# Optimization experiments

Measured on AMD Instinct MI355X. Metric: run time of the kernel, lower is better.

## Reference

```python
import jax, jax.numpy as jnp
import numpy as np

DIM = 1024
HEADS = 16
DIM_HEAD = 64
SCALE = DIM_HEAD ** -0.5
LN_EPS = 1e-5


def layer_norm(x, g, b):
    mu = jnp.mean(x, axis=-1, keepdims=True)
    var = jnp.mean(jnp.square(x - mu), axis=-1, keepdims=True)
    return (x - mu) * jax.lax.rsqrt(var + LN_EPS) * g + b


def setup_inputs() -> dict:
    key = jax.random.key(0)
    ks = jax.random.split(key, 8)
    w_std = DIM ** -0.5  # keep GEMM outputs O(1)
    return {
        "query": jax.random.normal(ks[0], (4, 512, DIM), jnp.float32),
        "kv": jax.random.normal(ks[1], (4, 2048, DIM), jnp.float32),
        "ln_q_g": jnp.ones((DIM,), jnp.float32),
        "ln_q_b": jnp.zeros((DIM,), jnp.float32),
        "ln_kv_g": jnp.ones((DIM,), jnp.float32),
        "ln_kv_b": jnp.zeros((DIM,), jnp.float32),
        "Wq": jax.random.normal(ks[2], (DIM, DIM), jnp.float32) * w_std,
        "bq": jnp.zeros((DIM,), jnp.float32),
        "Wk": jax.random.normal(ks[3], (DIM, DIM), jnp.float32) * w_std,
        "bk": jnp.zeros((DIM,), jnp.float32),
        "Wv": jax.random.normal(ks[4], (DIM, DIM), jnp.float32) * w_std,
        "bv": jnp.zeros((DIM,), jnp.float32),
        "Wo": jax.random.normal(ks[5], (DIM, DIM), jnp.float32) * w_std,
        "bo": jnp.zeros((DIM,), jnp.float32),
    }


def reference(query, kv, ln_q_g, ln_q_b, ln_kv_g, ln_kv_b,
              Wq, bq, Wk, bk, Wv, bv, Wo, bo):
    kv_n = layer_norm(kv, ln_kv_g, ln_kv_b)            # (b, n_kv, d)
    residual = query
    q_n = layer_norm(query, ln_q_g, ln_q_b)            # (b, n_q, d)

    q = q_n @ Wq + bq                                   # (b, n_q, inner)
    kv_input = jnp.concatenate((kv_n, q_n), axis=-2)    # (b, n_kv+n_q, d)
    k = kv_input @ Wk + bk
    v = kv_input @ Wv + bv

    def split_heads(t):
        b, n, _ = t.shape
        return t.reshape(b, n, HEADS, DIM_HEAD).transpose(0, 2, 1, 3)  # b h n dh

    q = split_heads(q) * SCALE
    k = split_heads(k)
    v = split_heads(v)

    sim = jnp.einsum('bhid,bhjd->bhij', q, k)           # (b, h, n_q, n_kv+n_q)
    sim = sim - jax.lax.stop_gradient(jnp.max(sim, axis=-1, keepdims=True))
    attn = jax.nn.softmax(sim, axis=-1)
    out = jnp.einsum('bhij,bhjd->bhid', attn, v)        # (b, h, n_q, dh)

    b, h, n, dh = out.shape
    out = out.transpose(0, 2, 1, 3).reshape(b, n, h * dh)
    return out @ Wo + bo + residual
```

## Files before the change

### kernel.cpp

```cpp
#include <hip/hip_runtime.h>
#include <hip/hip_bf16.h>

#define B_    4
#define NQ    512
#define NKV   2048
#define NT    2560
#define DIM_  1024
#define HEADS 16
#define DH    64
#define NSEQT 10240
#define SCALE_Q_L2E 0.18033688011112042f

typedef short bf16x8 __attribute__((ext_vector_type(8)));
typedef float f32x4  __attribute__((ext_vector_type(4)));
typedef __hip_bfloat16 bf16;

__device__ inline void gll16(const bf16* g, bf16* l) {
  __builtin_amdgcn_global_load_lds(
      (const __attribute__((address_space(1))) unsigned int*)g,
      (__attribute__((address_space(3))) unsigned int*)l, 16, 0, 0);
}

#define VMCNT(n) asm volatile("s_waitcnt vmcnt(" #n ")" ::: "memory")
#define BAR() __builtin_amdgcn_s_barrier()

__global__ __launch_bounds__(256) void prep_kernel(
    const float* __restrict__ query, const float* __restrict__ kv,
    const float* __restrict__ lgq, const float* __restrict__ lbq,
    const float* __restrict__ lgkv, const float* __restrict__ lbkv,
    bf16* __restrict__ X,
    const float* __restrict__ W0, const float* __restrict__ W1,
    const float* __restrict__ W2, const float* __restrict__ W3,
    bf16* __restrict__ T0, bf16* __restrict__ T1,
    bf16* __restrict__ T2, bf16* __restrict__ T3)
{
  __shared__ __align__(16) char psm[9216];
  const int t = threadIdx.x;
  const int blkid = blockIdx.x;
  if (blkid < B_*NT) {
    float* sh = (float*)psm;
    int b = blkid / NT, r = blkid % NT;
    const float *src, *g, *bb;
    if (r < NKV) { src = kv    + ((size_t)b*NKV + r)*DIM_;      g = lgkv; bb = lbkv; }
    else         { src = query + ((size_t)b*NQ + (r-NKV))*DIM_; g = lgq;  bb = lbq;  }
    float4 v = ((const float4*)src)[t];
    float s  = v.x+v.y+v.z+v.w;
    float s2 = v.x*v.x+v.y*v.y+v.z*v.z+v.w*v.w;
    #pragma unroll
    for (int m=1;m<64;m<<=1){ s += __shfl_xor(s,m,64); s2 += __shfl_xor(s2,m,64); }
    int wave=t>>6, lane=t&63;
    if(lane==0){ sh[wave]=s; sh[4+wave]=s2; }
    __syncthreads();
    s  = sh[0]+sh[1]+sh[2]+sh[3];
    s2 = sh[4]+sh[5]+sh[6]+sh[7];
    float mu = s*(1.0f/DIM_);
    float rs = rsqrtf(s2*(1.0f/DIM_) - mu*mu + 1e-5f);
    float4 gg = ((const float4*)g)[t];
    float4 b4 = ((const float4*)bb)[t];
    bf16* dst = X + (size_t)blkid*DIM_ + t*4;
    dst[0]=__float2bfloat16((v.x-mu)*rs*gg.x + b4.x);
    dst[1]=__float2bfloat16((v.y-mu)*rs*gg.y + b4.y);
    dst[2]=__float2bfloat16((v.z-mu)*rs*gg.z + b4.z);
    dst[3]=__float2bfloat16((v.w-mu)*rs*gg.w + b4.w);
  } else {
    int l = blkid - B_*NT;
    const float* W; bf16* Wt;
    switch (l>>8) {
      case 0: W=W0; Wt=T0; break;
      case 1: W=W1; Wt=T1; break;
      case 2: W=W2; Wt=T2; break;
      default: W=W3; Wt=T3; break;
    }
    int rem = l & 255;
    int k0 = (rem&15)*64, n0 = (rem>>4)*64;
    bf16* Ws = (bf16*)psm;
    int kr = t>>2, nseg = (t&3)*16;
    const float4* s4 = (const float4*)(W + (size_t)(k0+kr)*DIM_ + n0 + nseg);
    union { uint4 u[2]; bf16 h[16]; } pk;
    #pragma unroll
    for (int j=0;j<4;j++){
      float4 v = s4[j];
      pk.h[j*4+0]=__float2bfloat16(v.x); pk.h[j*4+1]=__float2bfloat16(v.y);
      pk.h[j*4+2]=__float2bfloat16(v.z); pk.h[j*4+3]=__float2bfloat16(v.w);
    }
    *(uint4*)(Ws + kr*72 + nseg)     = pk.u[0];
    *(uint4*)(Ws + kr*72 + nseg + 8) = pk.u[1];
    __syncthreads();
    int n = t&63, kseg = t>>6;
    union { uint4 u[2]; bf16 h[16]; } o;
    #pragma unroll
    for (int k=0;k<16;k++) o.h[k] = Ws[(kseg*16+k)*72 + n];
    bf16* dst = Wt + (size_t)(n0+n)*DIM_ + k0 + kseg*16;
    *(uint4*)dst = o.u[0];
    *(uint4*)(dst+8) = o.u[1];
  }
}

__device__ __forceinline__ void gemm_core2(
    const bf16* __restrict__ A, const bf16* __restrict__ Bmat,
    const float* __restrict__ bias, const float* __restrict__ residual,
    void* __restrict__ outv, int rows_per_batch, int row_offset,
    int a_batch_stride_rows, int n_seq, float scale,
    int emode, int m0, int n0, char* smem)
{
  char* const sA = smem;
  char* const sB = smem + 32768;
  float* Ts = (float*)smem;

  const int t = threadIdx.x;
  const int srow = t >> 3;
  const int gsw  = (t & 7) ^ (srow & 7);
  const bf16* pA[4]; const bf16* pB[4];
  #pragma unroll
  for (int c = 0; c < 4; ++c) {
    int gm = m0 + c*32 + srow;
    int bi = gm / rows_per_batch;
    pA[c] = A + ((size_t)bi*a_batch_stride_rows + row_offset
                 + (gm - bi*rows_per_batch))*(size_t)DIM_ + gsw*8;
    pB[c] = Bmat + (size_t)(n0 + c*32 + srow)*(size_t)DIM_ + gsw*8;
  }
  const int toff = t*16;

  const int wave = t>>6, lane = t&63, qq = lane>>4, mr = lane&15;
  const int wm = (wave>>1)*64, wn = (wave&1)*64;
  const int xq0 = (( qq    ) ^ (mr&7)) << 4;
  const int xq1 = ((4 + qq ) ^ (mr&7)) << 4;

  f32x4 acc[4][4] = {};

  #pragma unroll
  for (int c=0;c<4;++c) gll16(pA[c], (bf16*)(sA + c*4096 + toff));
  #pragma unroll
  for (int c=0;c<4;++c) gll16(pB[c], (bf16*)(sB + c*4096 + toff));
  VMCNT(0);
  BAR();

  for (int kt = 0; kt < 16; ++kt) {
    const int cb = (kt&1) << 14;
    const int nb = ((kt+1)&1) << 14;
    if (kt < 15) {
      const int ko = (kt+1)*64;
      #pragma unroll
      for (int c=0;c<4;++c) gll16(pA[c] + ko, (bf16*)(sA + nb + c*4096 + toff));
      #pragma unroll
      for (int c=0;c<4;++c) gll16(pB[c] + ko, (bf16*)(sB + nb + c*4096 + toff));
    }
    #pragma unroll
    for (int kh = 0; kh < 2; ++kh) {
      const int xq = kh ? xq1 : xq0;
      bf16x8 af[4], bfr[4];
      #pragma unroll
      for (int ms=0; ms<4; ++ms)
        af[ms]  = *(const bf16x8*)(sA + cb + (wm + ms*16 + mr)*128 + xq);
      #pragma unroll
      for (int ns=0; ns<4; ++ns)
        bfr[ns] = *(const bf16x8*)(sB + cb + (wn + ns*16 + mr)*128 + xq);
      __builtin_amdgcn_s_setprio(1);
      #pragma unroll
      for (int ms=0; ms<4; ++ms)
        #pragma unroll
        for (int ns=0; ns<4; ++ns)
          acc[ms][ns] = __builtin_amdgcn_mfma_f32_16x16x32_bf16(
              af[ms], bfr[ns], acc[ms][ns], 0,0,0);
      __builtin_amdgcn_s_setprio(0);
    }
    VMCNT(0);
    BAR();
  }
  __syncthreads();

  const int lr = t>>3, cs = (t&7)*16;
  for (int R=0; R<4; R++){
    if ((wave>>1) == (R>>1)) {
      #pragma unroll
      for (int ms2=0; ms2<2; ms2++){
        int ms = (R&1)*2 + ms2;
        #pragma unroll
        for (int ns=0; ns<4; ns++){
          int col = wn + ns*16 + mr;
          #pragma unroll
          for (int r=0;r<4;r++)
            Ts[(ms2*16 + qq*4 + r)*132 + col] = acc[ms][ns][r];
        }
      }
    }
    __syncthreads();
    float v[16];
    #pragma unroll
    for (int j=0;j<4;j++){
      float4 f = *(const float4*)(Ts + lr*132 + cs + j*4);
      v[j*4+0]=f.x; v[j*4+1]=f.y; v[j*4+2]=f.z; v[j*4+3]=f.w;
    }
    int gr = m0 + R*32 + lr;
    int gc = n0 + cs;
    if (emode == 0) {
      float* out = (float*)outv;
      size_t base = (size_t)gr*DIM_ + gc;
      #pragma unroll
      for (int j=0;j<4;j++){
        float4 bv = *(const float4*)(bias + gc + j*4);
        float4 rv = *(const float4*)(residual + base + j*4);
        float4 o4;
        o4.x = v[j*4+0] + bv.x + rv.x;
        o4.y = v[j*4+1] + bv.y + rv.y;
        o4.z = v[j*4+2] + bv.z + rv.z;
        o4.w = v[j*4+3] + bv.w + rv.w;
        *(float4*)(out + base + j*4) = o4;
      }
    } else if (emode == 1) {
      int bb = gr / rows_per_batch;
      int n  = gr - bb*rows_per_batch;
      int hh = gc>>6, dh = gc&63;
      bf16* out = (bf16*)outv + ((size_t)(bb*HEADS + hh)*n_seq + n)*DH + dh;
      union { uint4 u[2]; bf16 h[16]; } pk;
      #pragma unroll
      for (int j=0;j<16;j++) pk.h[j] = __float2bfloat16((v[j] + bias[gc+j])*scale);
      *(uint4*)out     = pk.u[0];
      *(uint4*)(out+8) = pk.u[1];
    } else {
      float bc = bias[gr];
      bf16* out = (bf16*)outv + (size_t)gr*NSEQT + gc;
      union { uint4 u[2]; bf16 h[16]; } pk;
      #pragma unroll
      for (int j=0;j<16;j++) pk.h[j] = __float2bfloat16(v[j] + bc);
      *(uint4*)out     = pk.u[0];
      *(uint4*)(out+8) = pk.u[1];
    }
    __syncthreads();
  }
}

__global__ __launch_bounds__(256) void gemm_qkv3(
    const bf16* __restrict__ X,
    const bf16* __restrict__ WtQ, const bf16* __restrict__ WtK,
    const bf16* __restrict__ WtV,
    const float* __restrict__ bq, const float* __restrict__ bk,
    const float* __restrict__ bv,
    bf16* __restrict__ Qhb, bf16* __restrict__ Khb, bf16* __restrict__ VTg)
{
  __shared__ __align__(16) char smem[65536];
  const int blk = blockIdx.x;
  if (blk < 128) {
    gemm_core2(X, WtQ, bq, nullptr, Qhb, NQ, NKV, NT, NQ, SCALE_Q_L2E, 1,
               (blk&15)*128, (blk>>4)*128, smem);
  } else if (blk < 768) {
    int l = blk - 128;
    gemm_core2(X, WtK, bk, nullptr, Khb, NT, 0, NT, NT, 1.0f, 1,
               (l%80)*128, (l/80)*128, smem);
  } else {
    int l = blk - 768;
    gemm_core2(WtV, X, bv, nullptr, VTg, DIM_, 0, DIM_, NSEQT, 1.0f, 2,
               (l/80)*128, (l%80)*128, smem);
  }
}

__global__ __launch_bounds__(256) void gemm_o(
    const bf16* __restrict__ Ctx, const bf16* __restrict__ WtO,
    const float* __restrict__ bo, const float* __restrict__ residual,
    float* __restrict__ out)
{
  __shared__ __align__(16) char smem[65536];
  const int blk = blockIdx.x;
  gemm_core2(Ctx, WtO, bo, residual, out, B_*NQ, 0, B_*NQ, NQ, 1.0f, 0,
             (blk&15)*128, (blk>>4)*128, smem);
}

__global__ __launch_bounds__(256) void attn7_kernel(
    const bf16* __restrict__ Qh, const bf16* __restrict__ Kh,
    const bf16* __restrict__ VTg, bf16* __restrict__ Ctx)
{
  __shared__ __align__(16) bf16 KV[3][8192];
  __shared__ __align__(16) unsigned int Ps[4][640];

  const int t = threadIdx.x, wave = t>>6, lane = t&63;
  const int qq = lane>>4, mr = lane&15;
  const int blk = blockIdx.x;
  const int bh = (blk&7)*8 + (blk>>6);
  const int q0 = ((blk>>3)&7)*64;
  const int b = bh>>4, h = bh&15;
  const int pair = wave>>1, kh = wave&1;
  const int qb = pair*32;

  const int sl = t>>2, sc = t&3;
  const int skey = 32*(sl>>5) + 2*(sl&15) + ((sl>>4)&1);
  const bf16* Kb  = Kh + (size_t)bh*NT*DH + (size_t)skey*DH + sc*8;
  const bf16* VbT = VTg + ((size_t)(h*DH) + sl)*NSEQT + (size_t)b*NT + sc*8;

  bf16x8 qf[2][2];
  #pragma unroll
  for (int mt=0; mt<2; mt++){
    const bf16* Qb = Qh + ((size_t)bh*NQ + q0 + qb + mt*16 + mr)*DH;
    qf[mt][0] = *(const bf16x8*)(Qb + qq*8);
    qf[mt][1] = *(const bf16x8*)(Qb + 32 + qq*8);
  }

  f32x4 o[2][4] = {};
  float l[2][4] = {};
  unsigned int* Pw = &Ps[wave][0];

  const int NIT = NT/64;

  #pragma unroll
  for (int p = 0; p < 2; ++p) {
    bf16* bp = &KV[p][0];
    const size_t kt = (size_t)p*64;
    gll16(Kb  + kt*DH,      bp + t*8);
    gll16(Kb  + kt*DH + 32, bp + 2048 + t*8);
    gll16(VbT + kt,         bp + 4096 + t*8);
    gll16(VbT + kt + 32,    bp + 6144 + t*8);
  }

  for (int it = 0; it < NIT; it++) {
    VMCNT(4);
    BAR();
    {
      int pt = (it + 2 <= NIT - 1) ? (it + 2) : (NIT - 1);
      size_t kt = (size_t)pt*64;
      bf16* bp = &KV[(it+2)%3][0];
      gll16(Kb  + kt*DH,      bp + t*8);
      gll16(Kb  + kt*DH + 32, bp + 2048 + t*8);
      gll16(VbT + kt,         bp + 4096 + t*8);
      gll16(VbT + kt + 32,    bp + 6144 + t*8);
    }
    const bf16* cbuf = &KV[it%3][0];

    bf16x8 kf[2][2];
    #pragma unroll
    for (int g=0; g<2; g++){
      kf[g][0] = *(const bf16x8*)(cbuf + (32*kh + 16*g + mr)*32 + qq*8);
      kf[g][1] = *(const bf16x8*)(cbuf + 2048 + (32*kh + 16*g + mr)*32 + qq*8);
    }
    f32x4 s[2][2];
    __builtin_amdgcn_s_setprio(1);
    #pragma unroll
    for (int mt=0; mt<2; mt++)
      #pragma unroll
      for (int g=0; g<2; g++){
        f32x4 z = {};
        z = __builtin_amdgcn_mfma_f32_16x16x32_bf16(qf[mt][0], kf[g][0], z, 0,0,0);
        z = __builtin_amdgcn_mfma_f32_16x16x32_bf16(qf[mt][1], kf[g][1], z, 0,0,0);
        s[mt][g] = z;
      }
    __builtin_amdgcn_s_setprio(0);
    bf16x8 vf[4];
    #pragma unroll
    for (int n2=0; n2<4; n2++)
      vf[n2] = *(const bf16x8*)(cbuf + 4096 + kh*2048 + (n2*16+mr)*32 + qq*8);

    #pragma unroll
    for (int mt=0; mt<2; mt++)
      #pragma unroll
      for (int r=0; r<4; r++){
        float e0 = __builtin_amdgcn_exp2f(s[mt][0][r]);
        float e1 = __builtin_amdgcn_exp2f(s[mt][1][r]);
        l[mt][r] += e0 + e1;
        unsigned a0 = __float_as_uint(e0) + 0x8000u;
        unsigned a1 = __float_as_uint(e1) + 0x8000u;
        Pw[(mt*16 + qq*4 + r)*20 + mr] = __builtin_amdgcn_perm(a1, a0, 0x07060302u);
      }
    asm volatile("s_waitcnt lgkmcnt(0)" ::: "memory");
    bf16x8 pa[2];
    #pragma unroll
    for (int mt=0; mt<2; mt++)
      pa[mt] = *(const bf16x8*)(Pw + (mt*16+mr)*20 + qq*4);
    __builtin_amdgcn_s_setprio(1);
    #pragma unroll
    for (int mt=0; mt<2; mt++)
      #pragma unroll
      for (int n2=0; n2<4; n2++)
        o[mt][n2] = __builtin_amdgcn_mfma_f32_16x16x32_bf16(pa[mt], vf[n2], o[mt][n2], 0,0,0);
    __builtin_amdgcn_s_setprio(0);
  }

  float lsum[2][4];
  #pragma unroll
  for (int mt=0; mt<2; mt++)
    #pragma unroll
    for (int r=0; r<4; r++){
      float v = l[mt][r];
      #pragma unroll
      for (int m=1;m<16;m<<=1) v += __shfl_xor(v, m, 16);
      lsum[mt][r] = v;
    }

  __syncthreads();
  float* Of  = (float*)&KV[0][0];
  float* lsh = (float*)&Ps[0][0];
  if (kh == 1) {
    #pragma unroll
    for (int mt=0; mt<2; mt++){
      #pragma unroll
      for (int n2=0; n2<4; n2++)
        #pragma unroll
        for (int r=0; r<4; r++)
          Of[(qb + mt*16 + qq*4 + r)*68 + n2*16 + mr] = o[mt][n2][r];
      if (mr == 0)
        #pragma unroll
        for (int r=0; r<4; r++)
          lsh[qb + mt*16 + qq*4 + r] = lsum[mt][r];
    }
  }
  __syncthreads();
  if (kh == 0) {
    #pragma unroll
    for (int mt=0; mt<2; mt++)
      #pragma unroll
      for (int r=0; r<4; r++){
        int row = qb + mt*16 + qq*4 + r;
        float rl = 1.0f / (lsum[mt][r] + lsh[row]);
        #pragma unroll
        for (int n2=0; n2<4; n2++){
          int idx = row*68 + n2*16 + mr;
          Of[idx] = (o[mt][n2][r] + Of[idx]) * rl;
        }
      }
  }
  __syncthreads();
  {
    int row = t>>2, seg = (t&3)*16;
    union { uint4 u[2]; bf16 hh[16]; } pkv;
    #pragma unroll
    for (int j=0;j<16;j++) pkv.hh[j] = __float2bfloat16(Of[row*68 + seg + j]);
    bf16* dst = Ctx + ((size_t)b*NQ + q0 + row)*DIM_ + h*DH + seg;
    *(uint4*)dst = pkv.u[0];
    *(uint4*)(dst+8) = pkv.u[1];
  }
}

extern "C" void kernel_launch(void* const* d_in, const int* in_sizes, int n_in,
                              void* d_out, int out_size, void* d_ws, size_t ws_size,
                              hipStream_t stream)
{
  const float* query  = (const float*)d_in[0];
  const float* kv     = (const float*)d_in[1];
  const float* ln_q_g = (const float*)d_in[2];
  const float* ln_q_b = (const float*)d_in[3];
  const float* ln_kv_g= (const float*)d_in[4];
  const float* ln_kv_b= (const float*)d_in[5];
  const float* Wq = (const float*)d_in[6];
  const float* bq = (const float*)d_in[7];
  const float* Wk = (const float*)d_in[8];
  const float* bk = (const float*)d_in[9];
  const float* Wv = (const float*)d_in[10];
  const float* bv = (const float*)d_in[11];
  const float* Wo = (const float*)d_in[12];
  const float* bo = (const float*)d_in[13];
  float* out = (float*)d_out;

  char* ws = (char*)d_ws;
  size_t off = 0;
  auto take = [&](size_t bytes)->char* {
    char* p = ws + off; off += (bytes + 255) & ~(size_t)255; return p;
  };
  bf16* X    = (bf16*)take((size_t)B_*NT*DIM_*2);
  bf16* Qhb  = (bf16*)take((size_t)B_*NQ*DIM_*2);
  bf16* Khb  = (bf16*)take((size_t)B_*NT*DIM_*2);
  bf16* VTg  = (bf16*)take((size_t)DIM_*NSEQT*2);
  bf16* Ctx  = (bf16*)take((size_t)B_*NQ*DIM_*2);
  bf16* WtQ  = (bf16*)take((size_t)DIM_*DIM_*2);
  bf16* WtK  = (bf16*)take((size_t)DIM_*DIM_*2);
  bf16* WtV  = (bf16*)take((size_t)DIM_*DIM_*2);
  bf16* WtO  = (bf16*)take((size_t)DIM_*DIM_*2);

  prep_kernel<<<B_*NT + 1024, 256, 0, stream>>>(
      query, kv, ln_q_g, ln_q_b, ln_kv_g, ln_kv_b, X,
      Wq, Wk, Wv, Wo, WtQ, WtK, WtV, WtO);

  gemm_qkv3<<<1408, 256, 0, stream>>>(X, WtQ, WtK, WtV, bq, bk, bv,
                                      Qhb, Khb, VTg);

  attn7_kernel<<<512, 256, 0, stream>>>(Qhb, Khb, VTg, Ctx);

  gemm_o<<<128, 256, 0, stream>>>(Ctx, WtO, bo, query, out);
}
```

Before: 238.8 us.

## Use one wave per LayerNorm row and register-staged padded LDS in attention

The LayerNorm prep now handles one row per wave, four rows per block. This drops the block-level shared-memory reduction and barrier, and writes packed bf16 pairs. The attention kernel replaces its triple-buffered global_load_lds pipeline with register-staged double buffering. Data goes into padded LDS rows (72-byte stride) to cut bank conflicts on the K/V fragment reads. The trade-off is that prefetch depth drops from two tiles ahead to one, and register pressure rises from holding the next tile.

Measured after the change: 305.9 us. 28.1% more time.

```diff
diff --git a/kernel.cpp b/kernel.cpp
--- a/kernel.cpp
+++ b/kernel.cpp
@@ -24,7 +24,7 @@
 #define VMCNT(n) asm volatile("s_waitcnt vmcnt(" #n ")" ::: "memory")
 #define BAR() __builtin_amdgcn_s_barrier()
 
-__global__ __launch_bounds__(256) void prep_kernel(
+__global__ __launch_bounds__(256) void prep2_kernel(
     const float* __restrict__ query, const float* __restrict__ kv,
     const float* __restrict__ lgq, const float* __restrict__ lbq,
     const float* __restrict__ lgkv, const float* __restrict__ lbkv,
@@ -37,33 +37,40 @@
   __shared__ __align__(16) char psm[9216];
   const int t = threadIdx.x;
   const int blkid = blockIdx.x;
-  if (blkid < B_*NT) {
-    float* sh = (float*)psm;
-    int b = blkid / NT, r = blkid % NT;
-    const float *src, *g, *bb;
-    if (r < NKV) { src = kv    + ((size_t)b*NKV + r)*DIM_;      g = lgkv; bb = lbkv; }
-    else         { src = query + ((size_t)b*NQ + (r-NKV))*DIM_; g = lgq;  bb = lbq;  }
-    float4 v = ((const float4*)src)[t];
-    float s  = v.x+v.y+v.z+v.w;
-    float s2 = v.x*v.x+v.y*v.y+v.z*v.z+v.w*v.w;
+  if (blkid < 2560) {
+    const int w = t>>6, l = t&63;
+    const int R = blkid*4 + w;
+    int b = R / NT, r = R % NT;
+    const float *src, *gp, *bp;
+    if (r < NKV) { src = kv    + ((size_t)b*NKV + r)*DIM_;      gp = lgkv; bp = lbkv; }
+    else         { src = query + ((size_t)b*NQ + (r-NKV))*DIM_; gp = lgq;  bp = lbq;  }
+    float4 v[4];
+    #pragma unroll
+    for (int j=0;j<4;++j) v[j] = ((const float4*)src)[j*64 + l];
+    float s = 0.f, s2 = 0.f;
+    #pragma unroll
+    for (int j=0;j<4;++j){
+      s  += v[j].x+v[j].y+v[j].z+v[j].w;
+      s2 += v[j].x*v[j].x+v[j].y*v[j].y+v[j].z*v[j].z+v[j].w*v[j].w;
+    }
     #pragma unroll
     for (int m=1;m<64;m<<=1){ s += __shfl_xor(s,m,64); s2 += __shfl_xor(s2,m,64); }
-    int wave=t>>6, lane=t&63;
-    if(lane==0){ sh[wave]=s; sh[4+wave]=s2; }
-    __syncthreads();
-    s  = sh[0]+sh[1]+sh[2]+sh[3];
-    s2 = sh[4]+sh[5]+sh[6]+sh[7];
     float mu = s*(1.0f/DIM_);
     float rs = rsqrtf(s2*(1.0f/DIM_) - mu*mu + 1e-5f);
-    float4 gg = ((const float4*)g)[t];
-    float4 b4 = ((const float4*)bb)[t];
-    bf16* dst = X + (size_t)blkid*DIM_ + t*4;
-    dst[0]=__float2bfloat16((v.x-mu)*rs*gg.x + b4.x);
-    dst[1]=__float2bfloat16((v.y-mu)*rs*gg.y + b4.y);
-    dst[2]=__float2bfloat16((v.z-mu)*rs*gg.z + b4.z);
-    dst[3]=__float2bfloat16((v.w-mu)*rs*gg.w + b4.w);
+    uint2* drow = (uint2*)(X + (size_t)R*DIM_);
+    #pragma unroll
+    for (int j=0;j<4;++j){
+      float4 gg = ((const float4*)gp)[j*64 + l];
+      float4 b4 = ((const float4*)bp)[j*64 + l];
+      union { unsigned int u[2]; bf16 h[4]; } pk;
+      pk.h[0] = __float2bfloat16((v[j].x-mu)*rs*gg.x + b4.x);
+      pk.h[1] = __float2bfloat16((v[j].y-mu)*rs*gg.y + b4.y);
+      pk.h[2] = __float2bfloat16((v[j].z-mu)*rs*gg.z + b4.z);
+      pk.h[3] = __float2bfloat16((v[j].w-mu)*rs*gg.w + b4.w);
+      drow[j*64 + l] = make_uint2(pk.u[0], pk.u[1]);
+    }
   } else {
-    int l = blkid - B_*NT;
+    int l = blkid - 2560;
     const float* W; bf16* Wt;
     switch (l>>8) {
       case 0: W=W0; Wt=T0; break;
@@ -265,11 +272,11 @@
              (blk&15)*128, (blk>>4)*128, smem);
 }
 
-__global__ __launch_bounds__(256) void attn7_kernel(
+__global__ __launch_bounds__(256) void attn8_kernel(
     const bf16* __restrict__ Qh, const bf16* __restrict__ Kh,
     const bf16* __restrict__ VTg, bf16* __restrict__ Ctx)
 {
-  __shared__ __align__(16) bf16 KV[3][8192];
+  __shared__ __align__(16) char KVp[2][18432];
   __shared__ __align__(16) unsigned int Ps[4][640];
 
   const int t = threadIdx.x, wave = t>>6, lane = t&63;
@@ -285,6 +292,7 @@
   const int skey = 32*(sl>>5) + 2*(sl&15) + ((sl>>4)&1);
   const bf16* Kb  = Kh + (size_t)bh*NT*DH + (size_t)skey*DH + sc*8;
   const bf16* VbT = VTg + ((size_t)(h*DH) + sl)*NSEQT + (size_t)b*NT + sc*8;
+  const int wb = sl*72 + sc*16;
 
   bf16x8 qf[2][2];
   #pragma unroll
@@ -297,38 +305,35 @@
   f32x4 o[2][4] = {};
   float l[2][4] = {};
   unsigned int* Pw = &Ps[wave][0];
-
   const int NIT = NT/64;
 
-  #pragma unroll
-  for (int p = 0; p < 2; ++p) {
-    bf16* bp = &KV[p][0];
-    const size_t kt = (size_t)p*64;
-    gll16(Kb  + kt*DH,      bp + t*8);
-    gll16(Kb  + kt*DH + 32, bp + 2048 + t*8);
-    gll16(VbT + kt,         bp + 4096 + t*8);
-    gll16(VbT + kt + 32,    bp + 6144 + t*8);
+  {
+    uint4 r0 = *(const uint4*)(Kb);
+    uint4 r1 = *(const uint4*)(Kb + 32);
+    uint4 r2 = *(const uint4*)(VbT);
+    uint4 r3 = *(const uint4*)(VbT + 32);
+    char* bp = &KVp[0][0];
+    *(uint4*)(bp + wb)         = r0;
+    *(uint4*)(bp + 4608 + wb)  = r1;
+    *(uint4*)(bp + 9216 + wb)  = r2;
+    *(uint4*)(bp + 13824 + wb) = r3;
   }
 
   for (int it = 0; it < NIT; it++) {
-    VMCNT(4);
-    BAR();
-    {
-      int pt = (it + 2 <= NIT - 1) ? (it + 2) : (NIT - 1);
-      size_t kt = (size_t)pt*64;
-      bf16* bp = &KV[(it+2)%3][0];
-      gll16(Kb  + kt*DH,      bp + t*8);
-      gll16(Kb  + kt*DH + 32, bp + 2048 + t*8);
-      gll16(VbT + kt,         bp + 4096 + t*8);
-      gll16(VbT + kt + 32,    bp + 6144 + t*8);
-    }
-    const bf16* cbuf = &KV[it%3][0];
+    __syncthreads();
+    const int nt2 = ((it+1 < NIT) ? it+1 : NIT-1)*64;
+    uint4 r0 = *(const uint4*)(Kb + (size_t)nt2*DH);
+    uint4 r1 = *(const uint4*)(Kb + (size_t)nt2*DH + 32);
+    uint4 r2 = *(const uint4*)(VbT + nt2);
+    uint4 r3 = *(const uint4*)(VbT + nt2 + 32);
+
+    const char* cb = &KVp[it&1][0];
 
     bf16x8 kf[2][2];
     #pragma unroll
     for (int g=0; g<2; g++){
-      kf[g][0] = *(const bf16x8*)(cbuf + (32*kh + 16*g + mr)*32 + qq*8);
-      kf[g][1] = *(const bf16x8*)(cbuf + 2048 + (32*kh + 16*g + mr)*32 + qq*8);
+      kf[g][0] = *(const bf16x8*)(cb + (32*kh + 16*g + mr)*72 + qq*16);
+      kf[g][1] = *(const bf16x8*)(cb + 4608 + (32*kh + 16*g + mr)*72 + qq*16);
     }
     f32x4 s[2][2];
     __builtin_amdgcn_s_setprio(1);
@@ -345,7 +350,7 @@
     bf16x8 vf[4];
     #pragma unroll
     for (int n2=0; n2<4; n2++)
-      vf[n2] = *(const bf16x8*)(cbuf + 4096 + kh*2048 + (n2*16+mr)*32 + qq*8);
+      vf[n2] = *(const bf16x8*)(cb + 9216 + kh*4608 + (n2*16+mr)*72 + qq*16);
 
     #pragma unroll
     for (int mt=0; mt<2; mt++)
@@ -370,6 +375,14 @@
       for (int n2=0; n2<4; n2++)
         o[mt][n2] = __builtin_amdgcn_mfma_f32_16x16x32_bf16(pa[mt], vf[n2], o[mt][n2], 0,0,0);
     __builtin_amdgcn_s_setprio(0);
+
+    {
+      char* np = &KVp[(it+1)&1][0];
+      *(uint4*)(np + wb)         = r0;
+      *(uint4*)(np + 4608 + wb)  = r1;
+      *(uint4*)(np + 9216 + wb)  = r2;
+      *(uint4*)(np + 13824 + wb) = r3;
+    }
   }
 
   float lsum[2][4];
@@ -384,7 +397,7 @@
     }
 
   __syncthreads();
-  float* Of  = (float*)&KV[0][0];
+  float* Of  = (float*)&KVp[0][0];
   float* lsh = (float*)&Ps[0][0];
   if (kh == 1) {
     #pragma unroll
@@ -462,14 +475,14 @@
   bf16* WtV  = (bf16*)take((size_t)DIM_*DIM_*2);
   bf16* WtO  = (bf16*)take((size_t)DIM_*DIM_*2);
 
-  prep_kernel<<<B_*NT + 1024, 256, 0, stream>>>(
+  prep2_kernel<<<3584, 256, 0, stream>>>(
       query, kv, ln_q_g, ln_q_b, ln_kv_g, ln_kv_b, X,
       Wq, Wk, Wv, Wo, WtQ, WtK, WtV, WtO);
 
   gemm_qkv3<<<1408, 256, 0, stream>>>(X, WtQ, WtK, WtV, bq, bk, bv,
                                       Qhb, Khb, VTg);
 
-  attn7_kernel<<<512, 256, 0, stream>>>(Qhb, Khb, VTg, Ctx);
+  attn8_kernel<<<512, 256, 0, stream>>>(Qhb, Khb, VTg, Ctx);
 
   gemm_o<<<128, 256, 0, stream>>>(Ctx, WtO, bo, query, out);
 }
```
